# Performance work log

Measured on AMD Instinct MI355X. Metric: run time of the kernel, lower is better.

## Reference

```python
import jax, jax.numpy as jnp
import numpy as np

N_NODES = 100000
N_EDGES = 1600000
IN_FEATS = 128
N_HIDDEN = 128
N_CLASSES = 47


def setup_inputs() -> dict:
    key = jax.random.key(0)
    ks = jax.random.split(key, 12)
    def lin(k, fi, fo):
        s = 1.0 / np.sqrt(fi)
        return jax.random.uniform(k, (fi, fo), jnp.float32, -s, s)
    return {
        "x": jax.random.normal(ks[0], (N_NODES, IN_FEATS), jnp.float32),
        "src": jax.random.randint(ks[1], (N_EDGES,), 0, N_NODES, jnp.int32),
        "dst": jax.random.randint(ks[2], (N_EDGES,), 0, N_NODES, jnp.int32),
        "W_self0": lin(ks[3], IN_FEATS, N_HIDDEN),
        "W_neigh0": lin(ks[4], IN_FEATS, N_HIDDEN),
        "b0": jnp.zeros((N_HIDDEN,), jnp.float32),
        "W_self1": lin(ks[5], N_HIDDEN, N_HIDDEN),
        "W_neigh1": lin(ks[6], N_HIDDEN, N_HIDDEN),
        "b1": jnp.zeros((N_HIDDEN,), jnp.float32),
        "W_self2": lin(ks[7], N_HIDDEN, N_CLASSES),
        "W_neigh2": lin(ks[8], N_HIDDEN, N_CLASSES),
        "b2": jnp.zeros((N_CLASSES,), jnp.float32),
    }


def _sage_layer(h, src, dst, W_self, W_neigh, b):
    # DGL SAGEConv 'mean': fc_self(h_dst) + fc_neigh(mean of in-neighbor feats) + bias
    agg = jax.ops.segment_sum(h[src], dst, num_segments=N_NODES)  # [N, d]
    deg = jax.ops.segment_sum(jnp.ones((src.shape[0],), h.dtype), dst,
                              num_segments=N_NODES)
    h_neigh = agg / jnp.maximum(deg, 1.0)[:, None]
    return h @ W_self + h_neigh @ W_neigh + b


def reference(x, src, dst, W_self0, W_neigh0, b0, W_self1, W_neigh1, b1,
              W_self2, W_neigh2, b2):
    h = _sage_layer(x, src, dst, W_self0, W_neigh0, b0)
    h = jax.nn.relu(h)
    h = _sage_layer(h, src, dst, W_self1, W_neigh1, b1)
    h = jax.nn.relu(h)
    h = _sage_layer(h, src, dst, W_self2, W_neigh2, b2)
    return h
```

## Files before the change

### kernel.cpp

```cpp
#include <hip/hip_runtime.h>

#define NN 100000
#define NE 1600000
#define NBK 391
#define CHUNK 8192
#define NBLK ((NE + CHUNK - 1) / CHUNK)
#define MPAD 100096
#define CASTB 12500
#define PREPB (CASTB + 128 + 128 + 48)
#define GBLK 2048
#define NPW ((NN + 8191) / 8192)

using bf16x8 = __attribute__((ext_vector_type(8))) short;
using f32x4  = __attribute__((ext_vector_type(4))) float;

static __device__ __forceinline__ unsigned short f2bf(float f) {
    unsigned int u = __float_as_uint(f);
    unsigned int r = (u + 0x7FFFu + ((u >> 16) & 1u)) >> 16;
    return (unsigned short)r;
}
static __device__ __forceinline__ float lo16(unsigned int u) {
    return __uint_as_float(u << 16);
}
static __device__ __forceinline__ float hi16(unsigned int u) {
    return __uint_as_float(u & 0xFFFF0000u);
}
static __device__ __forceinline__ unsigned int pk(float lo, float hi) {
    return ((unsigned int)f2bf(hi) << 16) | (unsigned int)f2bf(lo);
}


__global__ __launch_bounds__(256) void k_hist_prep(
        const int* __restrict__ dst, int* __restrict__ ghist,
        const float4* __restrict__ x4, ushort4* __restrict__ XB4,
        const float* __restrict__ Ws0, const float* __restrict__ Wn0,
        unsigned short* __restrict__ BT0,
        const float* __restrict__ Ws1, const float* __restrict__ Wn1,
        unsigned short* __restrict__ BT1,
        const float* __restrict__ Ws2, const float* __restrict__ Wn2,
        unsigned short* __restrict__ BT2) {
    __shared__ int h[NBK];
    int bid = blockIdx.x, t = threadIdx.x;
    if (bid < NBLK) {
        for (int i = t; i < NBK; i += 256) h[i] = 0;
        __syncthreads();
        int beg = bid * CHUNK, end = min(beg + CHUNK, NE);
        for (int i = beg + t; i < end; i += 256)
            atomicAdd(&h[dst[i] >> 8], 1);
        __syncthreads();
        for (int i = t; i < NBK; i += 256) ghist[bid * NBK + i] = h[i];
        return;
    }
    int pb = bid - NBLK;
    if (pb < CASTB) {
        int i = pb * 256 + t;
        float4 v = x4[i];
        ushort4 o;
        o.x = f2bf(v.x); o.y = f2bf(v.y); o.z = f2bf(v.z); o.w = f2bf(v.w);
        XB4[i] = o;
    } else if (pb < CASTB + 128) {
        int idx = (pb - CASTB) * 256 + t;
        int k = idx >> 7, n = idx & 127;
        float v = (k < 128) ? Ws0[k * 128 + n] : Wn0[(k - 128) * 128 + n];
        BT0[n * 256 + k] = f2bf(v);
    } else if (pb < CASTB + 256) {
        int idx = (pb - CASTB - 128) * 256 + t;
        int k = idx >> 7, n = idx & 127;
        float v = (k < 128) ? Ws1[k * 128 + n] : Wn1[(k - 128) * 128 + n];
        BT1[n * 256 + k] = f2bf(v);
    } else {
        int idx = (pb - CASTB - 256) * 256 + t;
        if (idx < 96 * 128) {
            int n = idx >> 7, k = idx & 127;
            float v = 0.f;
            if (n < 48) { if (n < 47) v = Ws2[k * 47 + n]; }
            else        { int cc = n - 48; if (cc < 47) v = Wn2[k * 47 + cc]; }
            BT2[n * 128 + k] = f2bf(v);
        }
    }
}

__global__ __launch_bounds__(512) void k_basescan(const int* __restrict__ ghist,
                                                  int* __restrict__ boff,
                                                  int* __restrict__ gbase) {
    __shared__ int s[512];
    int t = threadIdx.x;
    int tot = 0;
    if (t < NBK) {
#pragma unroll 4
        for (int blk = 0; blk < NBLK; ++blk) tot += ghist[blk * NBK + t];
    }
    s[t] = tot;
    __syncthreads();
    for (int o = 1; o < 512; o <<= 1) {
        int u = (t >= o) ? s[t - o] : 0;
        __syncthreads();
        s[t] += u;
        __syncthreads();
    }
    int base = s[t] - tot;
    if (t <= NBK) boff[t] = base;
    if (t < NBK) {
        int run = base;
        for (int blk = 0; blk < NBLK; ++blk) {
            int g = ghist[blk * NBK + t];
            gbase[blk * NBK + t] = run;
            run += g;
        }
    }
}

__global__ __launch_bounds__(256) void k_scatter(const int* __restrict__ src,
                                                 const int* __restrict__ dst,
                                                 const int* __restrict__ gbase,
                                                 unsigned int* __restrict__ eb) {
    __shared__ int cur[NBK];
    int b = blockIdx.x, t = threadIdx.x;
    for (int i = t; i < NBK; i += 256) cur[i] = gbase[b * NBK + i];
    __syncthreads();
    int beg = b * CHUNK, end = min(beg + CHUNK, NE);
    for (int i = beg + t; i < end; i += 256) {
        int d = dst[i];
        int p = atomicAdd(&cur[d >> 8], 1);
        eb[p] = ((unsigned int)(d & 255) << 24) | (unsigned int)src[i];
    }
}

__global__ __launch_bounds__(256) void k_csr(const unsigned int* __restrict__ eb,
                                             const int* __restrict__ boff,
                                             int* __restrict__ rp,
                                             int* __restrict__ col) {
    __shared__ int h[256];
    __shared__ int sc[256];
    __shared__ int cur[256];
    int b = blockIdx.x, t = threadIdx.x;
    h[t] = 0;
    __syncthreads();
    int beg = boff[b], end = boff[b + 1];
    for (int e = beg + t; e < end; e += 256)
        atomicAdd(&h[eb[e] >> 24], 1);
    __syncthreads();
    int c = h[t];
    sc[t] = c;
    __syncthreads();
    for (int o = 1; o < 256; o <<= 1) {
        int v = (t >= o) ? sc[t - o] : 0;
        __syncthreads();
        sc[t] += v;
        __syncthreads();
    }
    int excl = beg + sc[t] - c;
    int node = (b << 8) + t;
    if (node < NN) rp[node] = excl;
    if (node == NN - 1) rp[NN] = NE;
    cur[t] = excl;
    __syncthreads();
    for (int e = beg + t; e < end; e += 256) {
        unsigned int p = eb[e];
        int pos = atomicAdd(&cur[p >> 24], 1);
        col[pos] = (int)(p & 0xFFFFFFu);
    }
}


__global__ __launch_bounds__(256) void k_gather128(
        const uint4* __restrict__ hb4,
        const int* __restrict__ rp, const int* __restrict__ col,
        uint4* __restrict__ hnb4) {
    int wave = blockIdx.x * 4 + (threadIdx.x >> 6);
    int lane = threadIdx.x & 63;
    int q = lane >> 4, l16 = lane & 15;
    int n0 = wave * NPW;
    int n1 = min(n0 + NPW, NN);
    for (int node = n0; node < n1; ++node) {
        int beg = rp[node], end = rp[node + 1];
        float a0 = 0.f, a1 = 0.f, a2 = 0.f, a3 = 0.f;
        float a4 = 0.f, a5 = 0.f, a6 = 0.f, a7 = 0.f;
        float b0 = 0.f, b1 = 0.f, b2 = 0.f, b3 = 0.f;
        float b4 = 0.f, b5 = 0.f, b6 = 0.f, b7 = 0.f;
        int e = beg;
        for (; e + 8 <= end; e += 8) {
            int c0 = col[e + q];
            int c1 = col[e + 4 + q];
            uint4 v0 = hb4[(size_t)c0 * 16 + l16];
            uint4 v1 = hb4[(size_t)c1 * 16 + l16];
            a0 += lo16(v0.x); a1 += hi16(v0.x); a2 += lo16(v0.y); a3 += hi16(v0.y);
            a4 += lo16(v0.z); a5 += hi16(v0.z); a6 += lo16(v0.w); a7 += hi16(v0.w);
            b0 += lo16(v1.x); b1 += hi16(v1.x); b2 += lo16(v1.y); b3 += hi16(v1.y);
            b4 += lo16(v1.z); b5 += hi16(v1.z); b6 += lo16(v1.w); b7 += hi16(v1.w);
        }
        for (; e < end; e += 4) {
            if (e + q < end) {
                uint4 v = hb4[(size_t)col[e + q] * 16 + l16];
                a0 += lo16(v.x); a1 += hi16(v.x); a2 += lo16(v.y); a3 += hi16(v.y);
                a4 += lo16(v.z); a5 += hi16(v.z); a6 += lo16(v.w); a7 += hi16(v.w);
            }
        }
        float s0 = a0 + b0, s1 = a1 + b1, s2 = a2 + b2, s3 = a3 + b3;
        float s4 = a4 + b4, s5 = a5 + b5, s6 = a6 + b6, s7 = a7 + b7;
        s0 += __shfl_xor(s0, 16); s0 += __shfl_xor(s0, 32);
        s1 += __shfl_xor(s1, 16); s1 += __shfl_xor(s1, 32);
        s2 += __shfl_xor(s2, 16); s2 += __shfl_xor(s2, 32);
        s3 += __shfl_xor(s3, 16); s3 += __shfl_xor(s3, 32);
        s4 += __shfl_xor(s4, 16); s4 += __shfl_xor(s4, 32);
        s5 += __shfl_xor(s5, 16); s5 += __shfl_xor(s5, 32);
        s6 += __shfl_xor(s6, 16); s6 += __shfl_xor(s6, 32);
        s7 += __shfl_xor(s7, 16); s7 += __shfl_xor(s7, 32);
        if (q == 0) {
            float d = (float)(end - beg);
            float inv = (d > 0.f) ? 1.0f / d : 0.0f;
            uint4 o;
            o.x = pk(s0 * inv, s1 * inv);
            o.y = pk(s2 * inv, s3 * inv);
            o.z = pk(s4 * inv, s5 * inv);
            o.w = pk(s6 * inv, s7 * inv);
            hnb4[(size_t)node * 16 + l16] = o;
        }
    }
}


__global__ __launch_bounds__(256, 2) void k_mgemm(
        const unsigned short* __restrict__ A0,
        const unsigned short* __restrict__ A1,
        const unsigned short* __restrict__ BT,
        const float* __restrict__ bias,
        unsigned short* __restrict__ outB) {
    int t = threadIdx.x;
    int lane = t & 63, wid = t >> 6;
    int wm = wid >> 1, wn = wid & 1;
    int lr = lane & 15, lg = lane >> 4;
    int row0 = blockIdx.x * 128 + wm * 64;
    int colw = wn * 64;
    f32x4 zero = {0.f, 0.f, 0.f, 0.f};
    f32x4 acc[4][4];
#pragma unroll
    for (int a = 0; a < 4; ++a)
#pragma unroll
        for (int b = 0; b < 4; ++b) acc[a][b] = zero;

#pragma unroll
    for (int p = 0; p < 2; ++p) {
        const unsigned short* A = p ? A1 : A0;
        bf16x8 bReg[4][4];
#pragma unroll
        for (int nf = 0; nf < 4; ++nf)
#pragma unroll
            for (int ks = 0; ks < 4; ++ks)
                bReg[nf][ks] = *(const bf16x8*)&BT[(size_t)(colw + nf * 16 + lr) * 256 + p * 128 + ks * 32 + lg * 8];
#pragma unroll
        for (int mf = 0; mf < 4; ++mf) {
            const unsigned short* Ar = A + (size_t)(row0 + mf * 16 + lr) * 128;
            bf16x8 aReg[4];
#pragma unroll
            for (int ks = 0; ks < 4; ++ks)
                aReg[ks] = *(const bf16x8*)&Ar[ks * 32 + lg * 8];
#pragma unroll
            for (int ks = 0; ks < 4; ++ks)
#pragma unroll
                for (int nf = 0; nf < 4; ++nf)
                    acc[mf][nf] = __builtin_amdgcn_mfma_f32_16x16x32_bf16(
                        aReg[ks], bReg[nf][ks], acc[mf][nf], 0, 0, 0);
        }
    }
    __syncthreads();
#pragma unroll
    for (int nf = 0; nf < 4; ++nf) {
        int cidx = colw + nf * 16 + lr;
        float bb = bias[cidx];
#pragma unroll
        for (int mf = 0; mf < 4; ++mf) {
#pragma unroll
            for (int j = 0; j < 4; ++j) {
                int row = row0 + mf * 16 + lg * 4 + j;
                if (row < NN) {
                    float v = fmaxf(acc[mf][nf][j] + bb, 0.f);
                    outB[(size_t)row * 128 + cidx] = f2bf(v);
                }
            }
        }
    }
}


__global__ __launch_bounds__(256, 2) void k_mgemm47(
        const unsigned short* __restrict__ A,
        const unsigned short* __restrict__ BT2,
        const float* __restrict__ bias,
        float* __restrict__ S,
        unsigned short* __restrict__ TB) {
    int t = threadIdx.x;
    int lane = t & 63, wid = t >> 6;
    int wm = wid >> 1, wn = wid & 1;
    int lr = lane & 15, lg = lane >> 4;
    int row0 = blockIdx.x * 128 + wm * 64;
    int colw = wn * 48;
    f32x4 zero = {0.f, 0.f, 0.f, 0.f};
    f32x4 acc[4][3];
#pragma unroll
    for (int a = 0; a < 4; ++a)
#pragma unroll
        for (int b = 0; b < 3; ++b) acc[a][b] = zero;

    bf16x8 bReg[3][4];
#pragma unroll
    for (int nf = 0; nf < 3; ++nf)
#pragma unroll
        for (int ks = 0; ks < 4; ++ks)
            bReg[nf][ks] = *(const bf16x8*)&BT2[(size_t)(colw + nf * 16 + lr) * 128 + ks * 32 + lg * 8];
#pragma unroll
    for (int mf = 0; mf < 4; ++mf) {
        const unsigned short* Ar = A + (size_t)(row0 + mf * 16 + lr) * 128;
        bf16x8 aReg[4];
#pragma unroll
        for (int ks = 0; ks < 4; ++ks)
            aReg[ks] = *(const bf16x8*)&Ar[ks * 32 + lg * 8];
#pragma unroll
        for (int ks = 0; ks < 4; ++ks)
#pragma unroll
            for (int nf = 0; nf < 3; ++nf)
                acc[mf][nf] = __builtin_amdgcn_mfma_f32_16x16x32_bf16(
                    aReg[ks], bReg[nf][ks], acc[mf][nf], 0, 0, 0);
    }
#pragma unroll
    for (int nf = 0; nf < 3; ++nf) {
        int cidx = colw + nf * 16 + lr;
#pragma unroll
        for (int mf = 0; mf < 4; ++mf) {
#pragma unroll
            for (int j = 0; j < 4; ++j) {
                int row = row0 + mf * 16 + lg * 4 + j;
                if (row < NN) {
                    float v = acc[mf][nf][j];
                    if (cidx < 47)
                        S[(size_t)row * 48 + cidx] = v + bias[cidx];
                    else if (cidx >= 48)
                        TB[(size_t)row * 64 + (cidx - 48)] = f2bf(v);
                }
            }
        }
    }
}


__global__ __launch_bounds__(256) void k_gather47(
        const uint2* __restrict__ TB2,
        const float4* __restrict__ S4,
        const int* __restrict__ rp, const int* __restrict__ col,
        float* __restrict__ out) {
    int wave = blockIdx.x * 4 + (threadIdx.x >> 6);
    int lane = threadIdx.x & 63;
    int q = lane >> 4, l16 = lane & 15;
    int n0 = wave * NPW;
    int n1 = min(n0 + NPW, NN);
    for (int node = n0; node < n1; ++node) {
        int beg = rp[node], end = rp[node + 1];
        float a0 = 0.f, a1 = 0.f, a2 = 0.f, a3 = 0.f;
        float b0 = 0.f, b1 = 0.f, b2 = 0.f, b3 = 0.f;
        int e = beg;
        for (; e + 8 <= end; e += 8) {
            int i0 = col[e + q];
            int i1 = col[e + 4 + q];
            uint2 u0 = TB2[(size_t)i0 * 16 + l16];
            uint2 u1 = TB2[(size_t)i1 * 16 + l16];
            a0 += lo16(u0.x); a1 += hi16(u0.x); a2 += lo16(u0.y); a3 += hi16(u0.y);
            b0 += lo16(u1.x); b1 += hi16(u1.x); b2 += lo16(u1.y); b3 += hi16(u1.y);
        }
        for (; e < end; e += 4) {
            if (e + q < end) {
                uint2 u = TB2[(size_t)col[e + q] * 16 + l16];
                a0 += lo16(u.x); a1 += hi16(u.x); a2 += lo16(u.y); a3 += hi16(u.y);
            }
        }
        float s0 = a0 + b0, s1 = a1 + b1, s2 = a2 + b2, s3 = a3 + b3;
        s0 += __shfl_xor(s0, 16); s0 += __shfl_xor(s0, 32);
        s1 += __shfl_xor(s1, 16); s1 += __shfl_xor(s1, 32);
        s2 += __shfl_xor(s2, 16); s2 += __shfl_xor(s2, 32);
        s3 += __shfl_xor(s3, 16); s3 += __shfl_xor(s3, 32);
        if (q == 0 && l16 < 12) {
            float d = (float)(end - beg);
            float inv = (d > 0.f) ? 1.0f / d : 0.0f;
            float4 sv = S4[(size_t)node * 12 + l16];
            int c = l16 * 4;
            out[(size_t)node * 47 + c]     = sv.x + s0 * inv;
            out[(size_t)node * 47 + c + 1] = sv.y + s1 * inv;
            out[(size_t)node * 47 + c + 2] = sv.z + s2 * inv;
            if (c + 3 < 47) out[(size_t)node * 47 + c + 3] = sv.w + s3 * inv;
        }
    }
}


static inline size_t align_up(size_t x, size_t a) { return (x + a - 1) / a * a; }

extern "C" void kernel_launch(void* const* d_in, const int* in_sizes, int n_in,
                              void* d_out, int out_size, void* d_ws, size_t ws_size,
                              hipStream_t stream) {
    const float* x   = (const float*)d_in[0];
    const int* src   = (const int*)d_in[1];
    const int* dst   = (const int*)d_in[2];
    const float* Ws0 = (const float*)d_in[3];
    const float* Wn0 = (const float*)d_in[4];
    const float* b0  = (const float*)d_in[5];
    const float* Ws1 = (const float*)d_in[6];
    const float* Wn1 = (const float*)d_in[7];
    const float* b1  = (const float*)d_in[8];
    const float* Ws2 = (const float*)d_in[9];
    const float* Wn2 = (const float*)d_in[10];
    const float* b2  = (const float*)d_in[11];
    float* out = (float*)d_out;

    char* ws = (char*)d_ws;
    size_t off = 0;
    auto alloc = [&](size_t bytes) -> void* {
        void* p = ws + off; off = align_up(off + bytes, 256); return p;
    };
    int* row_ptr = (int*)alloc((size_t)(NN + 1) * 4);
    int* boff    = (int*)alloc((size_t)(NBK + 1) * 4);
    int* gbase   = (int*)alloc((size_t)NBLK * NBK * 4);
    int* ghist   = (int*)alloc((size_t)NBLK * NBK * 4);
    int* col     = (int*)alloc((size_t)NE * 4);
    unsigned short* XB  = (unsigned short*)alloc((size_t)MPAD * 128 * 2);
    unsigned short* BT0 = (unsigned short*)alloc(128 * 256 * 2);
    unsigned short* BT1 = (unsigned short*)alloc(128 * 256 * 2);
    unsigned short* BT2 = (unsigned short*)alloc(96 * 128 * 2);
    unsigned int* HNB   = (unsigned int*)alloc((size_t)MPAD * 128 * 2);
    size_t sbytes  = (size_t)NN * 48 * 4;
    size_t tbbytes = (size_t)MPAD * 64 * 2;
    char* stb = (char*)alloc(sbytes + tbbytes);
    unsigned int* eb   = (unsigned int*)stb;
    float* S           = (float*)stb;
    unsigned short* TB = (unsigned short*)(stb + sbytes);

    k_hist_prep<<<NBLK + PREPB, 256, 0, stream>>>(
        dst, ghist, (const float4*)x, (ushort4*)XB,
        Ws0, Wn0, BT0, Ws1, Wn1, BT1, Ws2, Wn2, BT2);
    k_basescan<<<1, 512, 0, stream>>>(ghist, boff, gbase);
    k_scatter<<<NBLK, 256, 0, stream>>>(src, dst, gbase, eb);
    k_csr<<<NBK, 256, 0, stream>>>(eb, boff, row_ptr, col);

    int mgrid = MPAD / 128;

    k_gather128<<<GBLK, 256, 0, stream>>>((const uint4*)XB, row_ptr, col, (uint4*)HNB);
    k_mgemm<<<mgrid, 256, 0, stream>>>(XB, (const unsigned short*)HNB, BT0, b0, XB);
    k_gather128<<<GBLK, 256, 0, stream>>>((const uint4*)XB, row_ptr, col, (uint4*)HNB);
    k_mgemm<<<mgrid, 256, 0, stream>>>(XB, (const unsigned short*)HNB, BT1, b1, XB);
    k_mgemm47<<<mgrid, 256, 0, stream>>>(XB, BT2, b2, S, TB);
    k_gather47<<<GBLK, 256, 0, stream>>>((const uint2*)TB, (const float4*)S,
                                         row_ptr, col, out);
}
```

Baseline: 354.6 us.

## Fuse neighbor gather with dense layer GEMM via per-wave LDS tiles

Replaces the separate gather kernel and two-input MFMA GEMM for the first two layers with one kernel. Each wave aggregates the mean of 16 nodes' neighbours, stages both self and neighbour rows in swizzled LDS, then runs the 16x256 by 256x128 product and writes the ReLU output. This removes the HNB intermediate round trip and one launch per layer, and ping-pongs between two feature buffers. In exchange each wave reloads the full weight matrix from global/L2 for every 16 rows, and 32KB of LDS per block may limit occupancy during the latency-bound gather.

Result: slower. 443.9 us (+25.2%).

```diff
diff --git a/kernel.cpp b/kernel.cpp
--- a/kernel.cpp
+++ b/kernel.cpp
@@ -10,6 +10,7 @@
 #define PREPB (CASTB + 128 + 128 + 48)
 #define GBLK 2048
 #define NPW ((NN + 8191) / 8192)
+#define FGBLK 1563
 
 using bf16x8 = __attribute__((ext_vector_type(8))) short;
 using f32x4  = __attribute__((ext_vector_type(4))) float;
@@ -163,120 +164,99 @@
 }
 
 
-__global__ __launch_bounds__(256) void k_gather128(
-        const uint4* __restrict__ hb4,
-        const int* __restrict__ rp, const int* __restrict__ col,
-        uint4* __restrict__ hnb4) {
-    int wave = blockIdx.x * 4 + (threadIdx.x >> 6);
-    int lane = threadIdx.x & 63;
-    int q = lane >> 4, l16 = lane & 15;
-    int n0 = wave * NPW;
-    int n1 = min(n0 + NPW, NN);
-    for (int node = n0; node < n1; ++node) {
-        int beg = rp[node], end = rp[node + 1];
-        float a0 = 0.f, a1 = 0.f, a2 = 0.f, a3 = 0.f;
-        float a4 = 0.f, a5 = 0.f, a6 = 0.f, a7 = 0.f;
-        float b0 = 0.f, b1 = 0.f, b2 = 0.f, b3 = 0.f;
-        float b4 = 0.f, b5 = 0.f, b6 = 0.f, b7 = 0.f;
-        int e = beg;
-        for (; e + 8 <= end; e += 8) {
-            int c0 = col[e + q];
-            int c1 = col[e + 4 + q];
-            uint4 v0 = hb4[(size_t)c0 * 16 + l16];
-            uint4 v1 = hb4[(size_t)c1 * 16 + l16];
-            a0 += lo16(v0.x); a1 += hi16(v0.x); a2 += lo16(v0.y); a3 += hi16(v0.y);
-            a4 += lo16(v0.z); a5 += hi16(v0.z); a6 += lo16(v0.w); a7 += hi16(v0.w);
-            b0 += lo16(v1.x); b1 += hi16(v1.x); b2 += lo16(v1.y); b3 += hi16(v1.y);
-            b4 += lo16(v1.z); b5 += hi16(v1.z); b6 += lo16(v1.w); b7 += hi16(v1.w);
-        }
-        for (; e < end; e += 4) {
-            if (e + q < end) {
-                uint4 v = hb4[(size_t)col[e + q] * 16 + l16];
-                a0 += lo16(v.x); a1 += hi16(v.x); a2 += lo16(v.y); a3 += hi16(v.y);
-                a4 += lo16(v.z); a5 += hi16(v.z); a6 += lo16(v.w); a7 += hi16(v.w);
-            }
-        }
-        float s0 = a0 + b0, s1 = a1 + b1, s2 = a2 + b2, s3 = a3 + b3;
-        float s4 = a4 + b4, s5 = a5 + b5, s6 = a6 + b6, s7 = a7 + b7;
-        s0 += __shfl_xor(s0, 16); s0 += __shfl_xor(s0, 32);
-        s1 += __shfl_xor(s1, 16); s1 += __shfl_xor(s1, 32);
-        s2 += __shfl_xor(s2, 16); s2 += __shfl_xor(s2, 32);
-        s3 += __shfl_xor(s3, 16); s3 += __shfl_xor(s3, 32);
-        s4 += __shfl_xor(s4, 16); s4 += __shfl_xor(s4, 32);
-        s5 += __shfl_xor(s5, 16); s5 += __shfl_xor(s5, 32);
-        s6 += __shfl_xor(s6, 16); s6 += __shfl_xor(s6, 32);
-        s7 += __shfl_xor(s7, 16); s7 += __shfl_xor(s7, 32);
-        if (q == 0) {
-            float d = (float)(end - beg);
-            float inv = (d > 0.f) ? 1.0f / d : 0.0f;
-            uint4 o;
-            o.x = pk(s0 * inv, s1 * inv);
-            o.y = pk(s2 * inv, s3 * inv);
-            o.z = pk(s4 * inv, s5 * inv);
-            o.w = pk(s6 * inv, s7 * inv);
-            hnb4[(size_t)node * 16 + l16] = o;
-        }
-    }
-}
-
-
-__global__ __launch_bounds__(256, 2) void k_mgemm(
-        const unsigned short* __restrict__ A0,
-        const unsigned short* __restrict__ A1,
+__global__ __launch_bounds__(256) void k_fgather(
+        const unsigned short* __restrict__ Ain,
         const unsigned short* __restrict__ BT,
         const float* __restrict__ bias,
-        unsigned short* __restrict__ outB) {
+        const int* __restrict__ rp, const int* __restrict__ col,
+        unsigned short* __restrict__ Aout) {
+    __shared__ char lds[32768];
     int t = threadIdx.x;
     int lane = t & 63, wid = t >> 6;
-    int wm = wid >> 1, wn = wid & 1;
-    int lr = lane & 15, lg = lane >> 4;
-    int row0 = blockIdx.x * 128 + wm * 64;
-    int colw = wn * 64;
+    int q = lane >> 4, l16 = lane & 15;
+    char* myl = lds + wid * 8192;
+    const uint4* hb4 = (const uint4*)Ain;
+    int base = (blockIdx.x * 4 + wid) * 16;
+
+    if (base < NN) {
+        for (int i = 0; i < 16; ++i) {
+            int node = base + i;
+            int beg = 0, end = 0;
+            if (node < NN) { beg = rp[node]; end = rp[node + 1]; }
+            if (q == 1) {
+                int srow = (node < NN) ? node : 0;
+                uint4 sv = hb4[(size_t)srow * 16 + l16];
+                *(uint4*)(myl + i * 512 + ((l16 * 16) ^ ((i & 7) << 4))) = sv;
+            }
+            float a0=0.f,a1=0.f,a2=0.f,a3=0.f,a4=0.f,a5=0.f,a6=0.f,a7=0.f;
+            float b0=0.f,b1=0.f,b2=0.f,b3=0.f,b4=0.f,b5=0.f,b6=0.f,b7=0.f;
+            int e = beg;
+            for (; e + 8 <= end; e += 8) {
+                int c0 = col[e + q];
+                int c1 = col[e + 4 + q];
+                uint4 v0 = hb4[(size_t)c0 * 16 + l16];
+                uint4 v1 = hb4[(size_t)c1 * 16 + l16];
+                a0 += lo16(v0.x); a1 += hi16(v0.x); a2 += lo16(v0.y); a3 += hi16(v0.y);
+                a4 += lo16(v0.z); a5 += hi16(v0.z); a6 += lo16(v0.w); a7 += hi16(v0.w);
+                b0 += lo16(v1.x); b1 += hi16(v1.x); b2 += lo16(v1.y); b3 += hi16(v1.y);
+                b4 += lo16(v1.z); b5 += hi16(v1.z); b6 += lo16(v1.w); b7 += hi16(v1.w);
+            }
+            for (; e < end; e += 4) {
+                if (e + q < end) {
+                    uint4 v = hb4[(size_t)col[e + q] * 16 + l16];
+                    a0 += lo16(v.x); a1 += hi16(v.x); a2 += lo16(v.y); a3 += hi16(v.y);
+                    a4 += lo16(v.z); a5 += hi16(v.z); a6 += lo16(v.w); a7 += hi16(v.w);
+                }
+            }
+            float s0 = a0 + b0, s1 = a1 + b1, s2 = a2 + b2, s3 = a3 + b3;
+            float s4 = a4 + b4, s5 = a5 + b5, s6 = a6 + b6, s7 = a7 + b7;
+            s0 += __shfl_xor(s0, 16); s0 += __shfl_xor(s0, 32);
+            s1 += __shfl_xor(s1, 16); s1 += __shfl_xor(s1, 32);
+            s2 += __shfl_xor(s2, 16); s2 += __shfl_xor(s2, 32);
+            s3 += __shfl_xor(s3, 16); s3 += __shfl_xor(s3, 32);
+            s4 += __shfl_xor(s4, 16); s4 += __shfl_xor(s4, 32);
+            s5 += __shfl_xor(s5, 16); s5 += __shfl_xor(s5, 32);
+            s6 += __shfl_xor(s6, 16); s6 += __shfl_xor(s6, 32);
+            s7 += __shfl_xor(s7, 16); s7 += __shfl_xor(s7, 32);
+            if (q == 0) {
+                float d = (float)(end - beg);
+                float inv = (d > 0.f) ? 1.0f / d : 0.0f;
+                uint4 o;
+                o.x = pk(s0 * inv, s1 * inv);
+                o.y = pk(s2 * inv, s3 * inv);
+                o.z = pk(s4 * inv, s5 * inv);
+                o.w = pk(s6 * inv, s7 * inv);
+                *(uint4*)(myl + i * 512 + ((256 + l16 * 16) ^ ((i & 7) << 4))) = o;
+            }
+        }
+    }
+    __syncthreads();
+    if (base >= NN) return;
+
+    int lr = l16, lg = q;
+    bf16x8 aReg[8];
+#pragma unroll
+    for (int ks = 0; ks < 8; ++ks)
+        aReg[ks] = *(const bf16x8*)(myl + lr * 512 + ((ks * 64 + lg * 16) ^ ((lr & 7) << 4)));
     f32x4 zero = {0.f, 0.f, 0.f, 0.f};
-    f32x4 acc[4][4];
-#pragma unroll
-    for (int a = 0; a < 4; ++a)
-#pragma unroll
-        for (int b = 0; b < 4; ++b) acc[a][b] = zero;
-
-#pragma unroll
-    for (int p = 0; p < 2; ++p) {
-        const unsigned short* A = p ? A1 : A0;
-        bf16x8 bReg[4][4];
-#pragma unroll
-        for (int nf = 0; nf < 4; ++nf)
-#pragma unroll
-            for (int ks = 0; ks < 4; ++ks)
-                bReg[nf][ks] = *(const bf16x8*)&BT[(size_t)(colw + nf * 16 + lr) * 256 + p * 128 + ks * 32 + lg * 8];
-#pragma unroll
-        for (int mf = 0; mf < 4; ++mf) {
-            const unsigned short* Ar = A + (size_t)(row0 + mf * 16 + lr) * 128;
-            bf16x8 aReg[4];
-#pragma unroll
-            for (int ks = 0; ks < 4; ++ks)
-                aReg[ks] = *(const bf16x8*)&Ar[ks * 32 + lg * 8];
-#pragma unroll
-            for (int ks = 0; ks < 4; ++ks)
-#pragma unroll
-                for (int nf = 0; nf < 4; ++nf)
-                    acc[mf][nf] = __builtin_amdgcn_mfma_f32_16x16x32_bf16(
-                        aReg[ks], bReg[nf][ks], acc[mf][nf], 0, 0, 0);
-        }
-    }
-    __syncthreads();
-#pragma unroll
-    for (int nf = 0; nf < 4; ++nf) {
-        int cidx = colw + nf * 16 + lr;
+#pragma unroll
+    for (int ct = 0; ct < 8; ++ct) {
+        bf16x8 bReg[8];
+#pragma unroll
+        for (int ks = 0; ks < 8; ++ks)
+            bReg[ks] = *(const bf16x8*)&BT[(size_t)(ct * 16 + lr) * 256 + ks * 32 + lg * 8];
+        f32x4 acc = zero;
+#pragma unroll
+        for (int ks = 0; ks < 8; ++ks)
+            acc = __builtin_amdgcn_mfma_f32_16x16x32_bf16(aReg[ks], bReg[ks], acc, 0, 0, 0);
+        int cidx = ct * 16 + lr;
         float bb = bias[cidx];
 #pragma unroll
-        for (int mf = 0; mf < 4; ++mf) {
-#pragma unroll
-            for (int j = 0; j < 4; ++j) {
-                int row = row0 + mf * 16 + lg * 4 + j;
-                if (row < NN) {
-                    float v = fmaxf(acc[mf][nf][j] + bb, 0.f);
-                    outB[(size_t)row * 128 + cidx] = f2bf(v);
-                }
+        for (int j = 0; j < 4; ++j) {
+            int row = base + lg * 4 + j;
+            if (row < NN) {
+                float v = fmaxf(acc[j] + bb, 0.f);
+                Aout[(size_t)row * 128 + cidx] = f2bf(v);
             }
         }
     }
@@ -420,11 +400,11 @@
     int* gbase   = (int*)alloc((size_t)NBLK * NBK * 4);
     int* ghist   = (int*)alloc((size_t)NBLK * NBK * 4);
     int* col     = (int*)alloc((size_t)NE * 4);
-    unsigned short* XB  = (unsigned short*)alloc((size_t)MPAD * 128 * 2);
+    unsigned short* XB0 = (unsigned short*)alloc((size_t)MPAD * 128 * 2);
+    unsigned short* XB1 = (unsigned short*)alloc((size_t)MPAD * 128 * 2);
     unsigned short* BT0 = (unsigned short*)alloc(128 * 256 * 2);
     unsigned short* BT1 = (unsigned short*)alloc(128 * 256 * 2);
     unsigned short* BT2 = (unsigned short*)alloc(96 * 128 * 2);
-    unsigned int* HNB   = (unsigned int*)alloc((size_t)MPAD * 128 * 2);
     size_t sbytes  = (size_t)NN * 48 * 4;
     size_t tbbytes = (size_t)MPAD * 64 * 2;
     char* stb = (char*)alloc(sbytes + tbbytes);
@@ -433,19 +413,15 @@
     unsigned short* TB = (unsigned short*)(stb + sbytes);
 
     k_hist_prep<<<NBLK + PREPB, 256, 0, stream>>>(
-        dst, ghist, (const float4*)x, (ushort4*)XB,
+        dst, ghist, (const float4*)x, (ushort4*)XB0,
         Ws0, Wn0, BT0, Ws1, Wn1, BT1, Ws2, Wn2, BT2);
     k_basescan<<<1, 512, 0, stream>>>(ghist, boff, gbase);
     k_scatter<<<NBLK, 256, 0, stream>>>(src, dst, gbase, eb);
     k_csr<<<NBK, 256, 0, stream>>>(eb, boff, row_ptr, col);
 
-    int mgrid = MPAD / 128;
-
-    k_gather128<<<GBLK, 256, 0, stream>>>((const uint4*)XB, row_ptr, col, (uint4*)HNB);
-    k_mgemm<<<mgrid, 256, 0, stream>>>(XB, (const unsigned short*)HNB, BT0, b0, XB);
-    k_gather128<<<GBLK, 256, 0, stream>>>((const uint4*)XB, row_ptr, col, (uint4*)HNB);
-    k_mgemm<<<mgrid, 256, 0, stream>>>(XB, (const unsigned short*)HNB, BT1, b1, XB);
-    k_mgemm47<<<mgrid, 256, 0, stream>>>(XB, BT2, b2, S, TB);
+    k_fgather<<<FGBLK, 256, 0, stream>>>(XB0, BT0, b0, row_ptr, col, XB1);
+    k_fgather<<<FGBLK, 256, 0, stream>>>(XB1, BT1, b1, row_ptr, col, XB0);
+    k_mgemm47<<<MPAD / 128, 256, 0, stream>>>(XB0, BT2, b2, S, TB);
     k_gather47<<<GBLK, 256, 0, stream>>>((const uint2*)TB, (const float4*)S,
                                          row_ptr, col, out);
 }
```
